# Performance work log

Hardware: AMD Instinct MI355X
Metric: run time of the kernel (lower is better)

## Reference

```python
import jax, jax.numpy as jnp
import numpy as np

D_MODEL = 1024
NHEAD = 16
HEAD_DIM = D_MODEL // NHEAD
ROPE_BASE = 10000.0


def rotate_half(x):
    h = x.shape[-1] // 2
    return jnp.concatenate((-x[..., h:], x[..., :h]), axis=-1)


def rope_cos_sin(seq_len, dim, dtype):
    inv_freq = 1.0 / (ROPE_BASE ** (jnp.arange(0, dim, 2, dtype=jnp.float32) / dim))
    t = jnp.arange(seq_len, dtype=jnp.float32)
    freqs = jnp.einsum('i,j->ij', t, inv_freq)  # [S, dim/2]
    emb = jnp.concatenate((freqs, freqs), axis=-1)  # [S, dim]
    return jnp.cos(emb).astype(dtype), jnp.sin(emb).astype(dtype)


def setup_inputs() -> dict:
    key = jax.random.key(0)
    ks = jax.random.split(key, 9)
    b, s = 2, 2048
    lim = 1.0 / np.sqrt(D_MODEL)
    def lin(kw, kb):
        W = jax.random.uniform(kw, (D_MODEL, D_MODEL), jnp.float32, -lim, lim)
        bia = jax.random.uniform(kb, (D_MODEL,), jnp.float32, -lim, lim)
        return W, bia
    Wq, bq = lin(ks[0], ks[1])
    Wk, bk = lin(ks[2], ks[3])
    Wv, bv = lin(ks[4], ks[5])
    Wo, bo = lin(ks[6], ks[7])
    x = jax.random.normal(ks[8], (b, s, D_MODEL), jnp.float32)
    return {"x": x, "Wq": Wq, "bq": bq, "Wk": Wk, "bk": bk,
            "Wv": Wv, "bv": bv, "Wo": Wo, "bo": bo}


def reference(x, Wq, bq, Wk, bk, Wv, bv, Wo, bo):
    b, s, _ = x.shape
    scale = jnp.sqrt(jnp.asarray(HEAD_DIM, x.dtype))
    # projections (torch Linear: y = x @ W.T + b)
    q = x @ Wq.T + bq
    k = x @ Wk.T + bk
    v = x @ Wv.T + bv
    # [b, h, s, d]
    def split_heads(t):
        return t.reshape(b, s, NHEAD, HEAD_DIM).transpose(0, 2, 1, 3)
    q, k, v = split_heads(q), split_heads(k), split_heads(v)
    cos, sin = rope_cos_sin(s, HEAD_DIM, x.dtype)  # [s, d]
    q = q * cos + rotate_half(q) * sin
    k = k * cos + rotate_half(k) * sin
    scores = jnp.einsum('bhqd,bhkd->bhqk', q, k) / scale
    probs = jax.nn.softmax(scores, axis=-1)
    out = jnp.einsum('bhqk,bhkd->bhqd', probs, v)
    out = out.transpose(0, 2, 1, 3).reshape(b, s, D_MODEL)
    return out @ Wo.T + bo
```

## Files before the change

kernel.cpp:

```cpp
#include <hip/hip_runtime.h>
#include <hip/hip_bf16.h>
#include <stdint.h>


typedef __attribute__((ext_vector_type(8))) short bf16x8;
typedef __attribute__((ext_vector_type(4))) float f32x4;
typedef __attribute__((ext_vector_type(16))) float f32x16;
typedef __attribute__((ext_vector_type(4))) short short4v;
typedef __attribute__((ext_vector_type(4))) float float4v;
typedef __attribute__((ext_vector_type(4))) unsigned uint32x4;

#define DEV __device__ __forceinline__

DEV short f2bf(float f) {
  union { float f; uint32_t u; } v; v.f = f;
  uint32_t r = (v.u + 0x7fffu + ((v.u >> 16) & 1u)) >> 16;
  return (short)(uint16_t)r;
}
DEV float bf2f(short b) {
  union { uint32_t u; float f; } v; v.u = ((uint32_t)(uint16_t)b) << 16;
  return v.f;
}
DEV unsigned cvtpk(float a, float b) {
  unsigned d;
  asm("v_cvt_pk_bf16_f32 %0, %1, %2" : "=v"(d) : "v"(a), "v"(b));
  return d;
}
DEV void gload16(const void* g, const void* l) {
  __builtin_amdgcn_global_load_lds((const __attribute__((address_space(1))) void*)g,
                                   (__attribute__((address_space(3))) void*)l, 16, 0, 0);
}

__global__ void convert_kernel(const float* __restrict__ x,
                               const float* __restrict__ wq, const float* __restrict__ wk,
                               const float* __restrict__ wv, const float* __restrict__ wo,
                               short* __restrict__ xb, short* __restrict__ wqb,
                               short* __restrict__ wkb, short* __restrict__ wvb,
                               short* __restrict__ wob,
                               float* __restrict__ ct, float* __restrict__ st) {
  const int idx = blockIdx.x * blockDim.x + threadIdx.x;
  if (idx >= 2097152) {
    const int i2 = idx - 2097152;
    const int t = i2 >> 5, j = i2 & 31;
    const float f = (float)t * exp2f(-(float)j * (13.287712379549449f / 32.f));
    ct[i2] = cosf(f);
    st[i2] = sinf(f);
    return;
  }
  const float* src; short* dst; int off;
  if (idx < 1048576)      { src = x;  dst = xb;  off = idx; }
  else if (idx < 1310720) { src = wq; dst = wqb; off = idx - 1048576; }
  else if (idx < 1572864) { src = wk; dst = wkb; off = idx - 1310720; }
  else if (idx < 1835008) { src = wv; dst = wvb; off = idx - 1572864; }
  else                    { src = wo; dst = wob; off = idx - 1835008; }
  float4v v = *(const float4v*)(src + (size_t)off * 4);
  short4v o;
  o[0] = f2bf(v[0]); o[1] = f2bf(v[1]); o[2] = f2bf(v[2]); o[3] = f2bf(v[3]);
  *(short4v*)(dst + (size_t)off * 4) = o;
}

template<bool FINAL>
__global__ __launch_bounds__(256, 2) void gemm_bt(
    const short* __restrict__ A,
    const short* __restrict__ W0, const short* __restrict__ W1, const short* __restrict__ W2,
    const float* __restrict__ b0, const float* __restrict__ b1, const float* __restrict__ b2,
    short* __restrict__ o0, short* __restrict__ o1, short* __restrict__ o2,
    float* __restrict__ of,
    const float* __restrict__ ct, const float* __restrict__ st) {
  constexpr int K = 1024;
  __shared__ short lds[2 * 128 * 64];
  short* As = lds;
  short* Ws = lds + 128 * 64;

  const int tid = threadIdx.x;
  const int lane = tid & 63;
  const int w = tid >> 6;
  const int wr = w >> 1, wc = w & 1;
  const int bn = blockIdx.x, bm = blockIdx.y, z = blockIdx.z;

  const short* Wt = (z == 0) ? W0 : (z == 1 ? W1 : W2);
  const float* bias = (z == 0) ? b0 : (z == 1 ? b1 : b2);
  short* ob = (z == 0) ? o0 : (z == 1 ? o1 : o2);

  const int lrow = lane >> 3;
  const int clog = 16 * ((lane & 7) ^ lrow);

  f32x4 acc[4][4] = {};
  const size_t arowbase = (size_t)(bm * 128) * K;
  const size_t wrowbase = (size_t)(bn * 128) * K;

  for (int kt = 0; kt < K / 64; ++kt) {
    __syncthreads();
#pragma unroll
    for (int i = 0; i < 4; ++i) {
      const int c = i * 4 + w;
      const int row = c * 8 + lrow;
      gload16(A + arowbase + (size_t)row * K + kt * 64 + (clog >> 1),
              (const char*)As + c * 1024);
      gload16(Wt + wrowbase + (size_t)row * K + kt * 64 + (clog >> 1),
              (const char*)Ws + c * 1024);
    }
    __syncthreads();
#pragma unroll
    for (int kk = 0; kk < 2; ++kk) {
      bf16x8 af[4], bf[4];
      const int kb = (kk * 32 + (lane >> 4) * 8) * 2;
#pragma unroll
      for (int mi = 0; mi < 4; ++mi) {
        const int row = wr * 64 + mi * 16 + (lane & 15);
        af[mi] = *(const bf16x8*)((const char*)As + row * 128 + (kb ^ ((row & 7) << 4)));
      }
#pragma unroll
      for (int ni = 0; ni < 4; ++ni) {
        const int row = wc * 64 + ni * 16 + (lane & 15);
        bf[ni] = *(const bf16x8*)((const char*)Ws + row * 128 + (kb ^ ((row & 7) << 4)));
      }
#pragma unroll
      for (int mi = 0; mi < 4; ++mi)
#pragma unroll
        for (int ni = 0; ni < 4; ++ni)
          acc[mi][ni] = __builtin_amdgcn_mfma_f32_16x16x32_bf16(af[mi], bf[ni], acc[mi][ni], 0, 0, 0);
    }
  }

  float bv[4];
#pragma unroll
  for (int ni = 0; ni < 4; ++ni)
    bv[ni] = bias[bn * 128 + wc * 64 + ni * 16 + (lane & 15)];

#pragma unroll
  for (int mi = 0; mi < 4; ++mi) {
#pragma unroll
    for (int r = 0; r < 4; ++r) {
      const int m = bm * 128 + wr * 64 + mi * 16 + (lane >> 4) * 4 + r;
      float v[4];
#pragma unroll
      for (int ni = 0; ni < 4; ++ni) v[ni] = acc[mi][ni][r] + bv[ni];
      if (!FINAL && z < 2) {
        const int s = m & 2047;
        const float sc = (z == 0) ? 0.18033688011f : 1.0f;
#pragma unroll
        for (int jj = 0; jj < 2; ++jj) {
          const int j = jj * 16 + (lane & 15);
          const float c = ct[s * 32 + j] * sc, sn = st[s * 32 + j] * sc;
          const float a = v[jj], bb = v[jj + 2];
          v[jj]     = a * c - bb * sn;
          v[jj + 2] = bb * c + a * sn;
        }
      }
#pragma unroll
      for (int ni = 0; ni < 4; ++ni) {
        const int n = bn * 128 + wc * 64 + ni * 16 + (lane & 15);
        if (FINAL) {
          of[(size_t)m * 1024 + n] = v[ni];
        } else {
          const int b = m >> 11, s = m & 2047, h = n >> 6, d = n & 63;
          ob[(((size_t)(b * 16 + h)) * 2048 + s) * 64 + d] = f2bf(v[ni]);
        }
      }
    }
  }
}

__global__ void vtrans_kernel(const short* __restrict__ v, short* __restrict__ vt) {
  __shared__ short t[64][72];
  const int bh = blockIdx.x, st0 = blockIdx.y * 64;
  const int tid = threadIdx.x;
#pragma unroll
  for (int i = 0; i < 2; ++i) {
    const int j = i * 256 + tid;
    const int row = j >> 3, c8 = (j & 7) * 8;
    *(bf16x8*)&t[row][c8] = *(const bf16x8*)(v + (((size_t)bh * 2048) + st0 + row) * 64 + c8);
  }
  __syncthreads();
#pragma unroll
  for (int i = 0; i < 2; ++i) {
    const int j = i * 256 + tid;
    const int dd = j >> 3, s8 = (j & 7) * 8;
    const int b16 = s8 & ~15;
    const int hi8 = (s8 >> 3) & 1;
    bf16x8 o;
#pragma unroll
    for (int e = 0; e < 8; ++e)
      o[e] = t[b16 + 4 * hi8 + (e & 3) + 8 * (e >> 2)][dd];
    *(bf16x8*)(vt + (((size_t)bh * 64) + dd) * 2048 + st0 + s8) = o;
  }
}

__global__ __launch_bounds__(256, 2) void attn_kernel(
    const short* __restrict__ q, const short* __restrict__ k,
    const short* __restrict__ vt, short* __restrict__ ao) {
  __shared__ float fm[4 * 2112];

  const int tid = threadIdx.x, lane = tid & 63, w = tid >> 6;
  const int wg = w & 1, g = w >> 1;
  const int hi = lane >> 5;
  const int bh = blockIdx.x, qt = blockIdx.y;

  const int qrow0 = qt * 128 + wg * 64 + (lane & 31);
  const short* qb = q + ((size_t)bh * 2048 + qrow0) * 64 + hi * 8;
  bf16x8 qf0[4], qf1[4];
#pragma unroll
  for (int m = 0; m < 4; ++m) {
    qf0[m] = *(const bf16x8*)(qb + 16 * m);
    qf1[m] = *(const bf16x8*)(qb + 32 * 64 + 16 * m);
  }

  f32x16 acc0[2] = {}, acc1[2] = {};
  float l0 = 0.f, l1 = 0.f;

  const short* kp = k + ((size_t)bh * 2048 + g * 1024 + (lane & 31)) * 64 + 8 * hi;
  const short* vp = vt + ((size_t)bh * 64 + (lane & 31)) * 2048 + g * 1024 + 8 * hi;

  bf16x8 kf[2][4];
#pragma unroll
  for (int t = 0; t < 2; ++t)
#pragma unroll
    for (int m = 0; m < 4; ++m)
      kf[t][m] = *(const bf16x8*)(kp + t * 2048 + 16 * m);
  kp += 4096;

  for (int j = 0; j < 16; ++j) {
    f32x16 stv0[2] = {}, stv1[2] = {};
#pragma unroll
    for (int t = 0; t < 2; ++t)
#pragma unroll
      for (int m = 0; m < 4; ++m) {
        stv0[t] = __builtin_amdgcn_mfma_f32_32x32x16_bf16(kf[t][m], qf0[m], stv0[t], 0, 0, 0);
        stv1[t] = __builtin_amdgcn_mfma_f32_32x32x16_bf16(kf[t][m], qf1[m], stv1[t], 0, 0, 0);
      }

    bf16x8 vv[2][2][2];
#pragma unroll
    for (int t = 0; t < 2; ++t)
#pragma unroll
      for (int sl = 0; sl < 2; ++sl)
#pragma unroll
        for (int db = 0; db < 2; ++db)
          vv[t][sl][db] = *(const bf16x8*)(vp + db * 65536 + 32 * t + 16 * sl);
    vp += 64;
    if (j < 15) {
#pragma unroll
      for (int t = 0; t < 2; ++t)
#pragma unroll
        for (int m = 0; m < 4; ++m)
          kf[t][m] = *(const bf16x8*)(kp + t * 2048 + 16 * m);
      kp += 4096;
    }

#pragma unroll
    for (int t = 0; t < 2; ++t) {
#pragma unroll
      for (int r = 0; r < 16; ++r) {
        const float p0 = __builtin_amdgcn_exp2f(stv0[t][r]);
        const float p1 = __builtin_amdgcn_exp2f(stv1[t][r]);
        stv0[t][r] = p0; l0 += p0;
        stv1[t][r] = p1; l1 += p1;
      }
      uint32x4 pu0[2], pu1[2];
#pragma unroll
      for (int sl = 0; sl < 2; ++sl)
#pragma unroll
        for (int jj = 0; jj < 4; ++jj) {
          pu0[sl][jj] = cvtpk(stv0[t][8 * sl + 2 * jj], stv0[t][8 * sl + 2 * jj + 1]);
          pu1[sl][jj] = cvtpk(stv1[t][8 * sl + 2 * jj], stv1[t][8 * sl + 2 * jj + 1]);
        }
#pragma unroll
      for (int sl = 0; sl < 2; ++sl) {
        const bf16x8 pv0 = __builtin_bit_cast(bf16x8, pu0[sl]);
        const bf16x8 pv1 = __builtin_bit_cast(bf16x8, pu1[sl]);
#pragma unroll
        for (int db = 0; db < 2; ++db) {
          acc0[db] = __builtin_amdgcn_mfma_f32_32x32x16_bf16(vv[t][sl][db], pv0, acc0[db], 0, 0, 0);
          acc1[db] = __builtin_amdgcn_mfma_f32_32x32x16_bf16(vv[t][sl][db], pv1, acc1[db], 0, 0, 0);
        }
      }
    }
  }

  l0 += __shfl_xor(l0, 32);
  l1 += __shfl_xor(l1, 32);

  float* fm0 = fm + (wg * 2 + 0) * 2112;
  float* fm1 = fm + (wg * 2 + 1) * 2112;
  if (g == 1) {
    fm0[lane] = l0;
    fm1[lane] = l1;
#pragma unroll
    for (int db = 0; db < 2; ++db)
#pragma unroll
      for (int r = 0; r < 16; ++r) {
        fm0[64 + (db * 16 + r) * 64 + lane] = acc0[db][r];
        fm1[64 + (db * 16 + r) * 64 + lane] = acc1[db][r];
      }
  }
  __syncthreads();

  if (g == 0) {
    const int b = bh >> 4, h = bh & 15;
#pragma unroll
    for (int s = 0; s < 2; ++s) {
      float* fmp = s ? fm1 : fm0;
      f32x16* accp = s ? acc1 : acc0;
      const float rl = 1.0f / ((s ? l1 : l0) + fmp[lane]);
      const int qrow = qrow0 + 32 * s;
      short* orow = ao + ((size_t)b * 2048 + qrow) * 1024 + h * 64;
#pragma unroll
      for (int db = 0; db < 2; ++db)
#pragma unroll
        for (int gq = 0; gq < 4; ++gq) {
          short4v o;
#pragma unroll
          for (int jj = 0; jj < 4; ++jj) {
            const int r = 4 * gq + jj;
            const float v1 = fmp[64 + (db * 16 + r) * 64 + lane];
            o[jj] = f2bf((accp[db][r] + v1) * rl);
          }
          *(short4v*)(orow + db * 32 + 8 * gq + 4 * hi) = o;
        }
    }
  }
}

extern "C" void kernel_launch(void* const* d_in, const int* in_sizes, int n_in,
                              void* d_out, int out_size, void* d_ws, size_t ws_size,
                              hipStream_t stream) {
  const float* x  = (const float*)d_in[0];
  const float* Wq = (const float*)d_in[1];
  const float* bq = (const float*)d_in[2];
  const float* Wk = (const float*)d_in[3];
  const float* bk = (const float*)d_in[4];
  const float* Wv = (const float*)d_in[5];
  const float* bv = (const float*)d_in[6];
  const float* Wo = (const float*)d_in[7];
  const float* bo = (const float*)d_in[8];
  float* out = (float*)d_out;

  char* ws = (char*)d_ws;
  short* xb  = (short*)(ws);
  short* wqb = (short*)(ws + 8388608);
  short* wkb = (short*)(ws + 10485760);
  short* wvb = (short*)(ws + 12582912);
  short* wob = (short*)(ws + 14680064);
  float* ct  = (float*)(ws + 16777216);
  float* st  = (float*)(ws + 17039360);
  short* qb  = (short*)(ws + 17301504);
  short* kb  = (short*)(ws + 25690112);
  short* vb  = (short*)(ws + 34078720);
  short* vtb = (short*)(ws + 42467328);
  short* ab  = (short*)(ws + 50855936);

  convert_kernel<<<dim3(8448), dim3(256), 0, stream>>>(
      x, Wq, Wk, Wv, Wo, xb, wqb, wkb, wvb, wob, ct, st);
  gemm_bt<false><<<dim3(8, 32, 3), dim3(256), 0, stream>>>(
      xb, wqb, wkb, wvb, bq, bk, bv, qb, kb, vb, (float*)nullptr, ct, st);
  vtrans_kernel<<<dim3(32, 32), dim3(256), 0, stream>>>(vb, vtb);
  attn_kernel<<<dim3(32, 16), dim3(256), 0, stream>>>(qb, kb, vtb, ab);
  gemm_bt<true><<<dim3(8, 32, 1), dim3(256), 0, stream>>>(
      ab, wob, (short*)nullptr, (short*)nullptr, bo, (float*)nullptr, (float*)nullptr,
      (short*)nullptr, (short*)nullptr, (short*)nullptr, out, ct, st);
}
```

Baseline: 130.2 us.

## Store K and V in MFMA fragment-major layout for coalesced attention loads

```diff
diff --git a/kernel.cpp b/kernel.cpp
--- a/kernel.cpp
+++ b/kernel.cpp
@@ -155,7 +155,15 @@
           of[(size_t)m * 1024 + n] = v[ni];
         } else {
           const int b = m >> 11, s = m & 2047, h = n >> 6, d = n & 63;
-          ob[(((size_t)(b * 16 + h)) * 2048 + s) * 64 + d] = f2bf(v[ni]);
+          const int bh = b * 16 + h;
+          if (z == 1) {
+            const size_t fi =
+                ((((((size_t)bh * 32 + (s >> 6)) * 2 + ((s >> 5) & 1)) * 4 + (d >> 4)) * 64
+                  + ((s & 31) + ((d >> 3) & 1) * 32)) * 8) + (d & 7);
+            ob[fi] = f2bf(v[ni]);
+          } else {
+            ob[(((size_t)bh) * 2048 + s) * 64 + d] = f2bf(v[ni]);
+          }
         }
       }
     }
@@ -183,13 +191,16 @@
 #pragma unroll
     for (int e = 0; e < 8; ++e)
       o[e] = t[b16 + 4 * hi8 + (e & 3) + 8 * (e >> 2)][dd];
-    *(bf16x8*)(vt + (((size_t)bh * 64) + dd) * 2048 + st0 + s8) = o;
+    const int kv0 = st0 + s8;
+    const int jg = kv0 >> 6, ts = (kv0 >> 4) & 3;
+    const int db = dd >> 5, ln = (dd & 31) + 32 * hi8;
+    *(bf16x8*)(vt + ((((size_t)bh * 32 + jg) * 4 + ts) * 2 + db) * 512 + ln * 8) = o;
   }
 }
 
 __global__ __launch_bounds__(256, 2) void attn_kernel(
-    const short* __restrict__ q, const short* __restrict__ k,
-    const short* __restrict__ vt, short* __restrict__ ao) {
+    const short* __restrict__ q, const short* __restrict__ kfb,
+    const short* __restrict__ vfb, short* __restrict__ ao) {
   __shared__ float fm[4 * 2112];
 
   const int tid = threadIdx.x, lane = tid & 63, w = tid >> 6;
@@ -209,15 +220,15 @@
   f32x16 acc0[2] = {}, acc1[2] = {};
   float l0 = 0.f, l1 = 0.f;
 
-  const short* kp = k + ((size_t)bh * 2048 + g * 1024 + (lane & 31)) * 64 + 8 * hi;
-  const short* vp = vt + ((size_t)bh * 64 + (lane & 31)) * 2048 + g * 1024 + 8 * hi;
+  const short* kp = kfb + (((size_t)bh * 32 + g * 16) * 8) * 512 + (size_t)lane * 8;
+  const short* vp = vfb + (((size_t)bh * 32 + g * 16) * 8) * 512 + (size_t)lane * 8;
 
   bf16x8 kf[2][4];
 #pragma unroll
   for (int t = 0; t < 2; ++t)
 #pragma unroll
     for (int m = 0; m < 4; ++m)
-      kf[t][m] = *(const bf16x8*)(kp + t * 2048 + 16 * m);
+      kf[t][m] = *(const bf16x8*)(kp + (t * 4 + m) * 512);
   kp += 4096;
 
   for (int j = 0; j < 16; ++j) {
@@ -237,14 +248,14 @@
       for (int sl = 0; sl < 2; ++sl)
 #pragma unroll
         for (int db = 0; db < 2; ++db)
-          vv[t][sl][db] = *(const bf16x8*)(vp + db * 65536 + 32 * t + 16 * sl);
-    vp += 64;
+          vv[t][sl][db] = *(const bf16x8*)(vp + ((t * 2 + sl) * 2 + db) * 512);
+    vp += 4096;
     if (j < 15) {
 #pragma unroll
       for (int t = 0; t < 2; ++t)
 #pragma unroll
         for (int m = 0; m < 4; ++m)
-          kf[t][m] = *(const bf16x8*)(kp + t * 2048 + 16 * m);
+          kf[t][m] = *(const bf16x8*)(kp + (t * 4 + m) * 512);
       kp += 4096;
     }
 
@@ -345,17 +356,17 @@
   float* ct  = (float*)(ws + 16777216);
   float* st  = (float*)(ws + 17039360);
   short* qb  = (short*)(ws + 17301504);
-  short* kb  = (short*)(ws + 25690112);
+  short* kfb = (short*)(ws + 25690112);
   short* vb  = (short*)(ws + 34078720);
-  short* vtb = (short*)(ws + 42467328);
+  short* vfb = (short*)(ws + 42467328);
   short* ab  = (short*)(ws + 50855936);
 
   convert_kernel<<<dim3(8448), dim3(256), 0, stream>>>(
       x, Wq, Wk, Wv, Wo, xb, wqb, wkb, wvb, wob, ct, st);
   gemm_bt<false><<<dim3(8, 32, 3), dim3(256), 0, stream>>>(
-      xb, wqb, wkb, wvb, bq, bk, bv, qb, kb, vb, (float*)nullptr, ct, st);
-  vtrans_kernel<<<dim3(32, 32), dim3(256), 0, stream>>>(vb, vtb);
-  attn_kernel<<<dim3(32, 16), dim3(256), 0, stream>>>(qb, kb, vtb, ab);
+      xb, wqb, wkb, wvb, bq, bk, bv, qb, kfb, vb, (float*)nullptr, ct, st);
+  vtrans_kernel<<<dim3(32, 32), dim3(256), 0, stream>>>(vb, vfb);
+  attn_kernel<<<dim3(32, 16), dim3(256), 0, stream>>>(qb, kfb, vfb, ab);
   gemm_bt<true><<<dim3(8, 32, 1), dim3(256), 0, stream>>>(
       ab, wob, (short*)nullptr, (short*)nullptr, bo, (float*)nullptr, (float*)nullptr,
       (short*)nullptr, (short*)nullptr, (short*)nullptr, out, ct, st);
```

After: 105.9 us. 18.6% less time.
